# Performance work log

Hardware: AMD Instinct MI355X
Metric: run time of the kernel (lower is better)

The kernel has to match this reference:

```python
import jax, jax.numpy as jnp
import numpy as np

NUM_CITIES = 128
NUM_ATTRS = 128
NUM_HIDDENS = 512
BATCH = 1024


def setup_inputs() -> dict:
    key = jax.random.key(0)
    ks = jax.random.split(key, 8)
    inp = {
        "input": jax.random.normal(ks[0], (BATCH, NUM_CITIES, NUM_ATTRS), dtype=jnp.float32),
        "state": jax.random.normal(ks[1], (BATCH, NUM_CITIES, NUM_HIDDENS), dtype=jnp.float32),
        "w_z": jax.random.normal(ks[2], (NUM_ATTRS, NUM_HIDDENS), dtype=jnp.float32) / 100.0,
        "u_z": jax.random.normal(ks[3], (NUM_HIDDENS, NUM_HIDDENS), dtype=jnp.float32) / 100.0,
        "b_z": jnp.zeros((NUM_HIDDENS,), dtype=jnp.float32),
        "w_r": jax.random.normal(ks[4], (NUM_ATTRS, NUM_HIDDENS), dtype=jnp.float32) / 100.0,
        "u_r": jax.random.normal(ks[5], (NUM_HIDDENS, NUM_HIDDENS), dtype=jnp.float32) / 100.0,
        "b_r": jnp.zeros((NUM_HIDDENS,), dtype=jnp.float32),
        "w_h": jax.random.normal(ks[6], (NUM_ATTRS, NUM_HIDDENS), dtype=jnp.float32) / 100.0,
        "u_h": jax.random.normal(ks[7], (NUM_HIDDENS, NUM_HIDDENS), dtype=jnp.float32) / 100.0,
        "b_h": jnp.zeros((NUM_HIDDENS,), dtype=jnp.float32),
    }
    return inp


def reference(input, state, w_z, u_z, b_z, w_r, u_r, b_r, w_h, u_h, b_h):
    # Flatten (batch, cities) into row dim, as the torch module does.
    x = input.reshape(-1, NUM_ATTRS)          # [B*C, A]
    h = state.reshape(-1, NUM_HIDDENS)        # [B*C, H]
    z = jax.nn.sigmoid(x @ w_z + h @ u_z + b_z)
    r = jax.nn.sigmoid(x @ w_r + h @ u_r + b_r)
    h_tilde = jnp.tanh(x @ w_h + (r * h) @ u_h + b_h)
    h_new = (1.0 - z) * h + z * h_tilde
    return h_new.reshape(-1, NUM_CITIES, NUM_HIDDENS)
```

## Files before the change

### kernel.cpp

```cpp
#include <hip/hip_runtime.h>
#include <cstdint>
#include <cstddef>


#define M_ROWS 131072
#define A_DIM 128
#define H_DIM 512
#define K_TOT 640
#define BK 32
#define NSTEPS 20
#define XSTEPS 4
#define BM 256
#define BN 128
#define SLOT_B 24576

typedef _Float16 f16;
typedef _Float16 f16x8 __attribute__((ext_vector_type(8)));
typedef float f32x4 __attribute__((ext_vector_type(4)));

#define AS1 __attribute__((address_space(1)))
#define AS3 __attribute__((address_space(3)))

__device__ __forceinline__ void gload_lds16(const void* g, void* l) {
  __builtin_amdgcn_global_load_lds((const AS1 unsigned int*)g,
                                   (AS3 unsigned int*)l, 16, 0, 0);
}

__device__ __forceinline__ float sigmoid_f(float v) {
  return __builtin_amdgcn_rcpf(1.0f + __expf(-v));
}
__device__ __forceinline__ float tanh_f(float v) {
  float c = fminf(fmaxf(v, -15.0f), 15.0f);
  float e = __expf(2.0f * c);
  return (e - 1.0f) * __builtin_amdgcn_rcpf(e + 1.0f);
}

#define NX8 (M_ROWS * A_DIM / 8)
#define NH8 (M_ROWS * H_DIM / 8)
#define NW  (1024 * K_TOT + H_DIM * K_TOT)

__global__ void prep_all(const float* __restrict__ x, const float* __restrict__ h,
                         const float* __restrict__ wz, const float* __restrict__ uz,
                         const float* __restrict__ wr, const float* __restrict__ ur,
                         const float* __restrict__ wh, const float* __restrict__ uh,
                         f16* __restrict__ x16, f16* __restrict__ h16,
                         f16* __restrict__ B1, f16* __restrict__ B2) {
  const long total = (long)NX8 + NH8 + NW;
  long i = (long)blockIdx.x * blockDim.x + threadIdx.x;
  const long stride = (long)gridDim.x * blockDim.x;
  for (; i < total; i += stride) {
    if (i < NX8 + NH8) {
      const float* src; f16* dst; long e;
      if (i < NX8) { src = x; dst = x16; e = i * 8; }
      else         { src = h; dst = h16; e = (i - NX8) * 8; }
      float4 v0 = *(const float4*)(src + e);
      float4 v1 = *(const float4*)(src + e + 4);
      f16x8 o;
      o[0] = (_Float16)v0.x; o[1] = (_Float16)v0.y; o[2] = (_Float16)v0.z; o[3] = (_Float16)v0.w;
      o[4] = (_Float16)v1.x; o[5] = (_Float16)v1.y; o[6] = (_Float16)v1.z; o[7] = (_Float16)v1.w;
      *(f16x8*)(dst + e) = o;
    } else {
      int idx = (int)(i - NX8 - NH8);
      const int n1 = 1024 * K_TOT;
      if (idx < n1) {
        int n = idx / K_TOT, k = idx % K_TOT;
        float v;
        if (k < A_DIM) v = (n < H_DIM) ? wz[k * H_DIM + n] : wr[k * H_DIM + (n - H_DIM)];
        else           v = (n < H_DIM) ? uz[(k - A_DIM) * H_DIM + n] : ur[(k - A_DIM) * H_DIM + (n - H_DIM)];
        B1[idx] = (f16)v;
      } else {
        int idx2 = idx - n1;
        int n = idx2 / K_TOT, k = idx2 % K_TOT;
        float v = (k < A_DIM) ? wh[k * H_DIM + n] : uh[(k - A_DIM) * H_DIM + n];
        B2[idx2] = (f16)v;
      }
    }
  }
}

__global__ void build_wcat(const float* __restrict__ wz, const float* __restrict__ uz,
                           const float* __restrict__ wr, const float* __restrict__ ur,
                           const float* __restrict__ wh, const float* __restrict__ uh,
                           f16* __restrict__ B1, f16* __restrict__ B2) {
  int idx = blockIdx.x * blockDim.x + threadIdx.x;
  const int n1 = 1024 * K_TOT;
  if (idx < n1) {
    int n = idx / K_TOT, k = idx % K_TOT;
    float v;
    if (k < A_DIM) v = (n < H_DIM) ? wz[k * H_DIM + n] : wr[k * H_DIM + (n - H_DIM)];
    else           v = (n < H_DIM) ? uz[(k - A_DIM) * H_DIM + n] : ur[(k - A_DIM) * H_DIM + (n - H_DIM)];
    B1[idx] = (f16)v;
  } else {
    int idx2 = idx - n1;
    if (idx2 < H_DIM * K_TOT) {
      int n = idx2 / K_TOT, k = idx2 % K_TOT;
      float v = (k < A_DIM) ? wh[k * H_DIM + n] : uh[(k - A_DIM) * H_DIM + n];
      B2[idx2] = (f16)v;
    }
  }
}

template <int MODE>
__global__ __launch_bounds__(512, 4)
void gru_gemm16p(const f16* __restrict__ A0, const f16* __restrict__ A1,
                 const f16* __restrict__ h16, const f16* __restrict__ Bt,
                 const float* __restrict__ bias0, const float* __restrict__ bias1,
                 float* __restrict__ out, f16* __restrict__ rh_out,
                 f16* __restrict__ z16) {
  constexpr int NBLK = (MODE == 1) ? 8 : 4;
  __shared__ __align__(16) char smem[3 * SLOT_B];

  const int per = gridDim.x >> 3;
  const int b = blockIdx.x;
  const int tile = (b & 7) * per + (b >> 3);
  const int nb = tile & (NBLK - 1);
  const int mb = tile / NBLK;
  const int m0 = mb * BM;
  const int n0 = nb * BN;

  const int tid = threadIdx.x;
  const int lane = tid & 63;
  const int wid = tid >> 6;
  const int wm = wid >> 1;
  const int wn = wid & 1;
  const int r16 = lane & 15;
  const int kh = lane >> 4;

  f32x4 acc[4][4];
#pragma unroll
  for (int i = 0; i < 4; ++i)
#pragma unroll
    for (int j = 0; j < 4; ++j) acc[i][j] = (f32x4){0.f, 0.f, 0.f, 0.f};

  auto dma_A = [&](int t, int slot) {
    char* Aw = smem + slot * SLOT_B;
    const f16* src = (t < XSTEPS) ? A0 : A1;
    const int ld = (t < XSTEPS) ? A_DIM : H_DIM;
    const int colb = (t < XSTEPS) ? t * BK : t * BK - A_DIM;
#pragma unroll
    for (int j = 0; j < 2; ++j) {
      const int s = j * 512 + tid;
      const int row = s >> 2;
      const int c = (s & 3) ^ ((row >> 1) & 3);
      const f16* g = src + (size_t)(m0 + row) * ld + colb + c * 8;
      gload_lds16(g, Aw + j * 8192 + wid * 1024);
    }
  };
  auto dma_B = [&](int t, int slot) {
    char* Bw = smem + slot * SLOT_B + 16384;
    const int s = tid;
    const int row = s >> 2;
    const int c = (s & 3) ^ ((row >> 1) & 3);
    const f16* g = Bt + (size_t)(n0 + row) * K_TOT + t * BK + c * 8;
    gload_lds16(g, Bw + wid * 1024);
  };

  dma_A(0, 0); dma_B(0, 0);
  dma_A(1, 1); dma_B(1, 1);

  int aoff[4], boff[4];
#pragma unroll
  for (int mi = 0; mi < 4; ++mi) {
    const int ra = wm * 64 + mi * 16 + r16;
    aoff[mi] = ra * 64 + ((kh ^ ((ra >> 1) & 3)) << 4);
  }
#pragma unroll
  for (int ni = 0; ni < 4; ++ni) {
    const int rb = wn * 64 + ni * 16 + r16;
    boff[ni] = 16384 + rb * 64 + ((kh ^ ((rb >> 1) & 3)) << 4);
  }

  for (int t = 0; t < NSTEPS; ++t) {
    if (t < NSTEPS - 1) asm volatile("s_waitcnt vmcnt(3)" ::: "memory");
    else                asm volatile("s_waitcnt vmcnt(0)" ::: "memory");
    __builtin_amdgcn_s_barrier();
    asm volatile("" ::: "memory");

    const char* Sl = smem + (t % 3) * SLOT_B;
    f16x8 aF[4], bF[4];
#pragma unroll
    for (int mi = 0; mi < 4; ++mi) aF[mi] = *(const f16x8*)(Sl + aoff[mi]);
#pragma unroll
    for (int ni = 0; ni < 4; ++ni) bF[ni] = *(const f16x8*)(Sl + boff[ni]);

    if (t + 2 < NSTEPS) {
      dma_A(t + 2, (t + 2) % 3);
      dma_B(t + 2, (t + 2) % 3);
    }

    asm volatile("s_waitcnt lgkmcnt(0)" ::: "memory");
    __builtin_amdgcn_s_setprio(1);
#pragma unroll
    for (int mi = 0; mi < 4; ++mi)
#pragma unroll
      for (int ni = 0; ni < 4; ++ni)
        acc[mi][ni] = __builtin_amdgcn_mfma_f32_16x16x32_f16(aF[mi], bF[ni], acc[mi][ni], 0, 0, 0);
    __builtin_amdgcn_s_setprio(0);
    asm volatile("" ::: "memory");
    __builtin_amdgcn_s_barrier();
    asm volatile("" ::: "memory");
  }

  const bool zhalf = (MODE == 1) && (n0 < H_DIM);
  float b4[4];
#pragma unroll
  for (int ni = 0; ni < 4; ++ni) {
    const int n_g = n0 + wn * 64 + ni * 16 + r16;
    b4[ni] = (MODE == 2) ? bias0[n_g] : (zhalf ? bias0[n_g] : bias1[n_g - H_DIM]);
  }
  __syncthreads();
  char* ep = smem;
#pragma unroll
  for (int mi = 0; mi < 4; ++mi) {
#pragma unroll
    for (int ni = 0; ni < 4; ++ni) {
      const int C = wn * 64 + ni * 16 + r16;
      const int sw = ((C >> 3) ^ (kh << 1)) << 4;
      const int cb = (C & 7) * 2;
#pragma unroll
      for (int r = 0; r < 4; ++r) {
        const int R = wm * 64 + mi * 16 + kh * 4 + r;
        const float v = acc[mi][ni][r] + b4[ni];
        const float a = (MODE == 2) ? tanh_f(v) : sigmoid_f(v);
        *(f16*)(ep + R * 256 + sw + cb) = (f16)a;
      }
    }
  }
  __syncthreads();

#pragma unroll
  for (int j = 0; j < 8; ++j) {
    const int sIdx = j * 512 + tid;
    const int R = sIdx >> 4;
    const int ss = sIdx & 15;
    const int sr = ss ^ (((R >> 2) & 3) << 1);
    const f16x8 tv = *(const f16x8*)(ep + R * 256 + sr * 16);
    const size_t m_g = (size_t)(m0 + R);
    if (MODE == 1) {
      if (zhalf) {
        const size_t off = m_g * H_DIM + n0 + ss * 8;
        if (z16) {
          *(f16x8*)(z16 + off) = tv;
        } else {
          float4 o0, o1;
          o0.x = (float)tv[0]; o0.y = (float)tv[1]; o0.z = (float)tv[2]; o0.w = (float)tv[3];
          o1.x = (float)tv[4]; o1.y = (float)tv[5]; o1.z = (float)tv[6]; o1.w = (float)tv[7];
          *(float4*)(out + off) = o0;
          *(float4*)(out + off + 4) = o1;
        }
      } else {
        const size_t off = m_g * H_DIM + (n0 - H_DIM) + ss * 8;
        const f16x8 hv = *(const f16x8*)(h16 + off);
        f16x8 rv;
#pragma unroll
        for (int e = 0; e < 8; ++e) rv[e] = (f16)((float)tv[e] * (float)hv[e]);
        *(f16x8*)(rh_out + off) = rv;
      }
    } else {
      const size_t off = m_g * H_DIM + n0 + ss * 8;
      const f16x8 hv = *(const f16x8*)(h16 + off);
      float zz[8];
      if (z16) {
        const f16x8 zv = *(const f16x8*)(z16 + off);
#pragma unroll
        for (int e = 0; e < 8; ++e) zz[e] = (float)zv[e];
      } else {
        const float4 z0 = *(const float4*)(out + off);
        const float4 z1 = *(const float4*)(out + off + 4);
        zz[0] = z0.x; zz[1] = z0.y; zz[2] = z0.z; zz[3] = z0.w;
        zz[4] = z1.x; zz[5] = z1.y; zz[6] = z1.z; zz[7] = z1.w;
      }
      float4 o0, o1;
      float oo[8];
#pragma unroll
      for (int e = 0; e < 8; ++e) {
        const float hh = (float)hv[e];
        oo[e] = fmaf(zz[e], (float)tv[e] - hh, hh);
      }
      o0.x = oo[0]; o0.y = oo[1]; o0.z = oo[2]; o0.w = oo[3];
      o1.x = oo[4]; o1.y = oo[5]; o1.z = oo[6]; o1.w = oo[7];
      *(float4*)(out + off) = o0;
      *(float4*)(out + off + 4) = o1;
    }
  }
}

template <int MODE>
__global__ __launch_bounds__(256, 2)
void gru_gemm_fb(const float* __restrict__ x, const float* __restrict__ h,
                 const f16* __restrict__ Bt, const f16* __restrict__ rh_in,
                 const float* __restrict__ bias0, const float* __restrict__ bias1,
                 float* __restrict__ out, f16* __restrict__ rh_out) {
  constexpr int NBLK = (MODE == 1) ? 8 : 4;
  __shared__ __align__(16) char smem[2 * 16384];

  const int per = gridDim.x >> 3;
  const int b = blockIdx.x;
  const int tile = (b & 7) * per + (b >> 3);
  const int nb = tile & (NBLK - 1);
  const int mb = tile / NBLK;
  const int m0 = mb * 128;
  const int n0 = nb * 128;

  const int tid = threadIdx.x;
  const int lane = tid & 63;
  const int wid = tid >> 6;
  const int wm = wid >> 1;
  const int wn = wid & 1;
  const int r16 = lane & 15;
  const int kh = lane >> 4;

  f32x4 acc[4][4];
#pragma unroll
  for (int i = 0; i < 4; ++i)
#pragma unroll
    for (int j = 0; j < 4; ++j) acc[i][j] = (f32x4){0.f, 0.f, 0.f, 0.f};

  float4 fa0, fa1, fa2, fa3;

  auto dma_B = [&](int t, int buf) {
    char* Bw = smem + buf * 16384 + 8192;
#pragma unroll
    for (int i = 0; i < 2; ++i) {
      const int chunk = wid * 2 + i;
      const int s = chunk * 64 + lane;
      const int row = s >> 2, c = s & 3;
      const f16* g = Bt + (size_t)(n0 + row) * K_TOT + t * BK + c * 8;
      gload_lds16(g, Bw + chunk * 1024);
    }
  };
  auto dma_A_rh = [&](int t, int buf) {
    char* Aw = smem + buf * 16384;
    const int col = t * BK - A_DIM;
#pragma unroll
    for (int i = 0; i < 2; ++i) {
      const int chunk = wid * 2 + i;
      const int s = chunk * 64 + lane;
      const int row = s >> 2, c = s & 3;
      const f16* g = rh_in + (size_t)(m0 + row) * H_DIM + col + c * 8;
      gload_lds16(g, Aw + chunk * 1024);
    }
  };
  auto load_A_regs = [&](int t) {
    const float* src = (t < XSTEPS) ? x : h;
    const int ld = (t < XSTEPS) ? A_DIM : H_DIM;
    const int col = (t < XSTEPS) ? t * BK : t * BK - A_DIM;
    {
      const int s = tid, row = s >> 2, c = s & 3;
      const float* g = src + (size_t)(m0 + row) * ld + col + c * 8;
      fa0 = *(const float4*)g;
      fa1 = *(const float4*)(g + 4);
    }
    {
      const int s = tid + 256, row = s >> 2, c = s & 3;
      const float* g = src + (size_t)(m0 + row) * ld + col + c * 8;
      fa2 = *(const float4*)g;
      fa3 = *(const float4*)(g + 4);
    }
  };
  auto write_A = [&](int buf) {
    char* Aw = smem + buf * 16384;
    f16x8 v;
    v[0] = (_Float16)fa0.x; v[1] = (_Float16)fa0.y; v[2] = (_Float16)fa0.z; v[3] = (_Float16)fa0.w;
    v[4] = (_Float16)fa1.x; v[5] = (_Float16)fa1.y; v[6] = (_Float16)fa1.z; v[7] = (_Float16)fa1.w;
    *(f16x8*)(Aw + tid * 16) = v;
    f16x8 w;
    w[0] = (_Float16)fa2.x; w[1] = (_Float16)fa2.y; w[2] = (_Float16)fa2.z; w[3] = (_Float16)fa2.w;
    w[4] = (_Float16)fa3.x; w[5] = (_Float16)fa3.y; w[6] = (_Float16)fa3.z; w[7] = (_Float16)fa3.w;
    *(f16x8*)(Aw + (tid + 256) * 16) = w;
  };

  dma_B(0, 0);
  load_A_regs(0);
  write_A(0);
  __syncthreads();

  int cur = 0;
  for (int t = 0; t < NSTEPS; ++t) {
    const int nxt = t + 1;
    const bool have = nxt < NSTEPS;
    const bool nxt_dma_A = (MODE == 2) && (nxt >= XSTEPS);
    if (have) {
      dma_B(nxt, cur ^ 1);
      if (nxt_dma_A) dma_A_rh(nxt, cur ^ 1);
      else load_A_regs(nxt);
    }
    const char* Al = smem + cur * 16384;
    const char* Bl = Al + 8192;
    f16x8 aF[4], bF[4];
#pragma unroll
    for (int mi = 0; mi < 4; ++mi)
      aF[mi] = *(const f16x8*)(Al + (wm * 64 + mi * 16 + r16) * 64 + kh * 16);
#pragma unroll
    for (int ni = 0; ni < 4; ++ni)
      bF[ni] = *(const f16x8*)(Bl + (wn * 64 + ni * 16 + r16) * 64 + kh * 16);
#pragma unroll
    for (int mi = 0; mi < 4; ++mi)
#pragma unroll
      for (int ni = 0; ni < 4; ++ni)
        acc[mi][ni] = __builtin_amdgcn_mfma_f32_16x16x32_f16(aF[mi], bF[ni], acc[mi][ni], 0, 0, 0);
    if (have && !nxt_dma_A) write_A(cur ^ 1);
    __syncthreads();
    cur ^= 1;
  }

#pragma unroll
  for (int mi = 0; mi < 4; ++mi) {
#pragma unroll
    for (int ni = 0; ni < 4; ++ni) {
      const int n_g = n0 + wn * 64 + ni * 16 + r16;
#pragma unroll
      for (int r = 0; r < 4; ++r) {
        const int m_g = m0 + wm * 64 + mi * 16 + kh * 4 + r;
        float v = acc[mi][ni][r];
        if (MODE == 1) {
          if (n_g < H_DIM) {
            out[(size_t)m_g * H_DIM + n_g] = sigmoid_f(v + bias0[n_g]);
          } else {
            const int j = n_g - H_DIM;
            const size_t off = (size_t)m_g * H_DIM + j;
            float rv = sigmoid_f(v + bias1[j]);
            rh_out[off] = (f16)(rv * h[off]);
          }
        } else {
          const size_t off = (size_t)m_g * H_DIM + n_g;
          float th = tanh_f(v + bias0[n_g]);
          float zv = out[off];
          float hv = h[off];
          out[off] = fmaf(zv, th - hv, hv);
        }
      }
    }
  }
}

extern "C" void kernel_launch(void* const* d_in, const int* in_sizes, int n_in,
                              void* d_out, int out_size, void* d_ws, size_t ws_size,
                              hipStream_t stream) {
  const float* x  = (const float*)d_in[0];
  const float* h  = (const float*)d_in[1];
  const float* wz = (const float*)d_in[2];
  const float* uz = (const float*)d_in[3];
  const float* bz = (const float*)d_in[4];
  const float* wr = (const float*)d_in[5];
  const float* ur = (const float*)d_in[6];
  const float* br = (const float*)d_in[7];
  const float* wh = (const float*)d_in[8];
  const float* uh = (const float*)d_in[9];
  const float* bh = (const float*)d_in[10];
  float* out = (float*)d_out;

  char* ws = (char*)d_ws;
  const size_t B1_B  = (size_t)1024 * K_TOT * 2;
  const size_t B2_B  = (size_t)H_DIM * K_TOT * 2;
  const size_t RH_B  = (size_t)M_ROWS * H_DIM * 2;
  const size_t X16_B = (size_t)M_ROWS * A_DIM * 2;
  const size_t H16_B = RH_B;
  const size_t Z16_B = RH_B;

  f16* B1 = (f16*)ws;
  f16* B2 = (f16*)(ws + B1_B);
  f16* rh = (f16*)(ws + B1_B + B2_B);

  const size_t need_base = B1_B + B2_B + RH_B + X16_B + H16_B;
  const int wtot = NW;

  if (ws_size >= need_base) {
    f16* x16 = (f16*)(ws + B1_B + B2_B + RH_B);
    f16* h16 = (f16*)(ws + B1_B + B2_B + RH_B + X16_B);
    f16* z16 = (ws_size >= need_base + Z16_B) ? (f16*)(ws + need_base) : nullptr;

    prep_all<<<dim3(2048), dim3(256), 0, stream>>>(
        x, h, wz, uz, wr, ur, wh, uh, x16, h16, B1, B2);
    gru_gemm16p<1><<<dim3((M_ROWS / BM) * 8), dim3(512), 0, stream>>>(
        x16, h16, h16, B1, bz, br, out, rh, z16);
    gru_gemm16p<2><<<dim3((M_ROWS / BM) * 4), dim3(512), 0, stream>>>(
        x16, rh, h16, B2, bh, nullptr, out, nullptr, z16);
  } else {
    build_wcat<<<dim3((wtot + 255) / 256), dim3(256), 0, stream>>>(wz, uz, wr, ur, wh, uh, B1, B2);
    gru_gemm_fb<1><<<dim3((M_ROWS / 128) * 8), dim3(256), 0, stream>>>(x, h, B1, nullptr, bz, br, out, rh);
    gru_gemm_fb<2><<<dim3((M_ROWS / 128) * 4), dim3(256), 0, stream>>>(x, h, B2, rh, bh, nullptr, out, rh);
  }
}
```

Baseline: 563.9 us.

## Load GEMM A operand directly into registers, keep only B staged in LDS

The A tiles (activations) are no longer DMA'd into a triple-buffered LDS slot. Each wave now reads its own 64 rows straight from global memory into registers, double-buffered one step ahead, while B keeps its LDS triple buffer. The trailing per-step barrier is dropped and the vmcnt waits are retuned to match. This cuts LDS traffic and one barrier per k-step, at the cost of redundant global A reads across waves that share rows, and global latency that is only hidden one step ahead.

```diff
diff --git a/kernel.cpp b/kernel.cpp
--- a/kernel.cpp
+++ b/kernel.cpp
@@ -12,7 +12,7 @@
 #define XSTEPS 4
 #define BM 256
 #define BN 128
-#define SLOT_B 24576
+#define BSLOT 8192
 
 typedef _Float16 f16;
 typedef _Float16 f16x8 __attribute__((ext_vector_type(8)));
@@ -102,13 +102,13 @@
 
 template <int MODE>
 __global__ __launch_bounds__(512, 4)
-void gru_gemm16p(const f16* __restrict__ A0, const f16* __restrict__ A1,
+void gru_gemm16a(const f16* __restrict__ A0, const f16* __restrict__ A1,
                  const f16* __restrict__ h16, const f16* __restrict__ Bt,
                  const float* __restrict__ bias0, const float* __restrict__ bias1,
                  float* __restrict__ out, f16* __restrict__ rh_out,
                  f16* __restrict__ z16) {
   constexpr int NBLK = (MODE == 1) ? 8 : 4;
-  __shared__ __align__(16) char smem[3 * SLOT_B];
+  __shared__ __align__(16) char smem[65536];
 
   const int per = gridDim.x >> 3;
   const int b = blockIdx.x;
@@ -132,22 +132,8 @@
 #pragma unroll
     for (int j = 0; j < 4; ++j) acc[i][j] = (f32x4){0.f, 0.f, 0.f, 0.f};
 
-  auto dma_A = [&](int t, int slot) {
-    char* Aw = smem + slot * SLOT_B;
-    const f16* src = (t < XSTEPS) ? A0 : A1;
-    const int ld = (t < XSTEPS) ? A_DIM : H_DIM;
-    const int colb = (t < XSTEPS) ? t * BK : t * BK - A_DIM;
-#pragma unroll
-    for (int j = 0; j < 2; ++j) {
-      const int s = j * 512 + tid;
-      const int row = s >> 2;
-      const int c = (s & 3) ^ ((row >> 1) & 3);
-      const f16* g = src + (size_t)(m0 + row) * ld + colb + c * 8;
-      gload_lds16(g, Aw + j * 8192 + wid * 1024);
-    }
-  };
   auto dma_B = [&](int t, int slot) {
-    char* Bw = smem + slot * SLOT_B + 16384;
+    char* Bw = smem + slot * BSLOT;
     const int s = tid;
     const int row = s >> 2;
     const int c = (s & 3) ^ ((row >> 1) & 3);
@@ -155,50 +141,56 @@
     gload_lds16(g, Bw + wid * 1024);
   };
 
-  dma_A(0, 0); dma_B(0, 0);
-  dma_A(1, 1); dma_B(1, 1);
-
-  int aoff[4], boff[4];
-#pragma unroll
-  for (int mi = 0; mi < 4; ++mi) {
-    const int ra = wm * 64 + mi * 16 + r16;
-    aoff[mi] = ra * 64 + ((kh ^ ((ra >> 1) & 3)) << 4);
-  }
+  int boff[4];
 #pragma unroll
   for (int ni = 0; ni < 4; ++ni) {
     const int rb = wn * 64 + ni * 16 + r16;
-    boff[ni] = 16384 + rb * 64 + ((kh ^ ((rb >> 1) & 3)) << 4);
-  }
-
-  for (int t = 0; t < NSTEPS; ++t) {
-    if (t < NSTEPS - 1) asm volatile("s_waitcnt vmcnt(3)" ::: "memory");
-    else                asm volatile("s_waitcnt vmcnt(0)" ::: "memory");
+    boff[ni] = rb * 64 + ((kh ^ ((rb >> 1) & 3)) << 4);
+  }
+
+  const int arow = m0 + wm * 64 + r16;
+  auto loadA = [&](int t, f16x8* aF) {
+    const f16* src = (t < XSTEPS) ? A0 : A1;
+    const int ld = (t < XSTEPS) ? A_DIM : H_DIM;
+    const int colb = ((t < XSTEPS) ? t * BK : t * BK - A_DIM) + kh * 8;
+#pragma unroll
+    for (int mi = 0; mi < 4; ++mi)
+      aF[mi] = *(const f16x8*)(src + (size_t)(arow + mi * 16) * ld + colb);
+  };
+
+  f16x8 aX[4], aY[4];
+
+  auto phase = [&](int t, const f16x8* aC, f16x8* aN) {
+    if (t == 0)              asm volatile("s_waitcnt vmcnt(1)" ::: "memory");
+    else if (t < NSTEPS - 1) asm volatile("s_waitcnt vmcnt(5)" ::: "memory");
+    else                     asm volatile("s_waitcnt vmcnt(4)" ::: "memory");
     __builtin_amdgcn_s_barrier();
     asm volatile("" ::: "memory");
-
-    const char* Sl = smem + (t % 3) * SLOT_B;
-    f16x8 aF[4], bF[4];
-#pragma unroll
-    for (int mi = 0; mi < 4; ++mi) aF[mi] = *(const f16x8*)(Sl + aoff[mi]);
-#pragma unroll
-    for (int ni = 0; ni < 4; ++ni) bF[ni] = *(const f16x8*)(Sl + boff[ni]);
-
-    if (t + 2 < NSTEPS) {
-      dma_A(t + 2, (t + 2) % 3);
-      dma_B(t + 2, (t + 2) % 3);
-    }
-
+    const char* Bl = smem + (t % 3) * BSLOT;
+    f16x8 bF[4];
+#pragma unroll
+    for (int ni = 0; ni < 4; ++ni) bF[ni] = *(const f16x8*)(Bl + boff[ni]);
+    if (t + 1 < NSTEPS) loadA(t + 1, aN);
+    if (t + 2 < NSTEPS) dma_B(t + 2, (t + 2) % 3);
     asm volatile("s_waitcnt lgkmcnt(0)" ::: "memory");
+    __builtin_amdgcn_sched_barrier(0);
     __builtin_amdgcn_s_setprio(1);
 #pragma unroll
     for (int mi = 0; mi < 4; ++mi)
 #pragma unroll
       for (int ni = 0; ni < 4; ++ni)
-        acc[mi][ni] = __builtin_amdgcn_mfma_f32_16x16x32_f16(aF[mi], bF[ni], acc[mi][ni], 0, 0, 0);
+        acc[mi][ni] = __builtin_amdgcn_mfma_f32_16x16x32_f16(aC[mi], bF[ni], acc[mi][ni], 0, 0, 0);
     __builtin_amdgcn_s_setprio(0);
     asm volatile("" ::: "memory");
-    __builtin_amdgcn_s_barrier();
-    asm volatile("" ::: "memory");
+  };
+
+  loadA(0, aX);
+  dma_B(0, 0);
+  dma_B(1, 1);
+
+  for (int t = 0; t < NSTEPS; t += 2) {
+    phase(t, aX, aY);
+    phase(t + 1, aY, aX);
   }
 
   const bool zhalf = (MODE == 1) && (n0 < H_DIM);
@@ -325,13 +317,13 @@
       const int chunk = wid * 2 + i;
       const int s = chunk * 64 + lane;
       const int row = s >> 2, c = s & 3;
-      const f16* g = Bt + (size_t)(n0 + row) * K_TOT + t * BK + c * 8;
+      const f16* g = Bt + (size_t)(n0 + row) * K_TOT + t * 32 + c * 8;
       gload_lds16(g, Bw + chunk * 1024);
     }
   };
   auto dma_A_rh = [&](int t, int buf) {
     char* Aw = smem + buf * 16384;
-    const int col = t * BK - A_DIM;
+    const int col = t * 32 - A_DIM;
 #pragma unroll
     for (int i = 0; i < 2; ++i) {
       const int chunk = wid * 2 + i;
@@ -344,7 +336,7 @@
   auto load_A_regs = [&](int t) {
     const float* src = (t < XSTEPS) ? x : h;
     const int ld = (t < XSTEPS) ? A_DIM : H_DIM;
-    const int col = (t < XSTEPS) ? t * BK : t * BK - A_DIM;
+    const int col = (t < XSTEPS) ? t * 32 : t * 32 - A_DIM;
     {
       const int s = tid, row = s >> 2, c = s & 3;
       const float* g = src + (size_t)(m0 + row) * ld + col + c * 8;
@@ -472,9 +464,9 @@
 
     prep_all<<<dim3(2048), dim3(256), 0, stream>>>(
         x, h, wz, uz, wr, ur, wh, uh, x16, h16, B1, B2);
-    gru_gemm16p<1><<<dim3((M_ROWS / BM) * 8), dim3(512), 0, stream>>>(
+    gru_gemm16a<1><<<dim3((M_ROWS / BM) * 8), dim3(512), 0, stream>>>(
         x16, h16, h16, B1, bz, br, out, rh, z16);
-    gru_gemm16p<2><<<dim3((M_ROWS / BM) * 4), dim3(512), 0, stream>>>(
+    gru_gemm16a<2><<<dim3((M_ROWS / BM) * 4), dim3(512), 0, stream>>>(
         x16, rh, h16, B2, bh, nullptr, out, nullptr, z16);
   } else {
     build_wcat<<<dim3((wtot + 255) / 256), dim3(256), 0, stream>>>(wz, uz, wr, ur, wh, uh, B1, B2);
```

New measurement: 836.4 us. 48.3% more time.
